# Performance work log

Measured on AMD Instinct MI355X. Metric: run time of the kernel, lower is better.

## Reference

```python
import jax, jax.numpy as jnp
import numpy as np

IN_C, OUT_C, P, K, STRIDE = 256, 256, 4, 3, 1
PAD = (K - 1) // 2

def setup_inputs() -> dict:
    key = jax.random.key(0)
    k1, k2, k3 = jax.random.split(key, 3)
    x = jax.random.normal(k1, (32, IN_C, 64, 64), dtype=jnp.float32)
    # KxK weights for (i,j) pairs where the KxK branch is taken
    Wk = jax.random.normal(k2, (OUT_C, IN_C, K, K), dtype=jnp.float32) * 0.05
    # 1x1 weights (one scalar per (i,j) pair) for the pointwise branch
    W1 = jax.random.normal(k3, (OUT_C, IN_C), dtype=jnp.float32) * 0.05
    return {"x": x, "Wk": Wk, "W1": W1}

def _effective_weight(Wk, W1):
    # Branch selection: j < first_K uses (in_c + j - first_K) % P == 0,
    # else (j - first_K) % P == 0; both equal (j - first_K) mod P == 0
    # with nonnegative modulo, where first_K = i % in_c.
    i = jnp.arange(OUT_C)[:, None]
    j = jnp.arange(IN_C)[None, :]
    first_K = i % IN_C
    kxk_mask = ((j - first_K) % P == 0)  # [out, in] bool
    # 1x1 conv (pad 0, stride s) == center tap of a padded KxK conv (pad (K-1)/2, stride s)
    center = jnp.zeros((K, K), Wk.dtype).at[K // 2, K // 2].set(1.0)
    W_1x1_embedded = W1[:, :, None, None] * center  # [out, in, K, K]
    return jnp.where(kxk_mask[:, :, None, None], Wk, W_1x1_embedded)

def reference(x, Wk, W1):
    W_eff = _effective_weight(Wk, W1)
    out = jax.lax.conv_general_dilated(
        x, W_eff,
        window_strides=(STRIDE, STRIDE),
        padding=[(PAD, PAD), (PAD, PAD)],
        dimension_numbers=("NCHW", "OIHW", "NCHW"),
    )
    return out
```

## Files before the change

kernel.cpp:

```cpp
#include <hip/hip_runtime.h>


#define IN_C  256
#define OUT_C 256
#define HH    64
#define WW    64

typedef __attribute__((ext_vector_type(8))) short   bf16x8;
typedef __attribute__((ext_vector_type(4))) float   f32x4;

__device__ __forceinline__ unsigned short f2bf(float f) {
    union { float f; unsigned int u; } v; v.f = f;
    unsigned int r = (v.u + 0x7FFFu + ((v.u >> 16) & 1u)) >> 16;
    return (unsigned short)r;
}

__global__ __launch_bounds__(256)
void hetconv_prep(const float* __restrict__ Wk, const float* __restrict__ W1,
                  unsigned short* __restrict__ ws16) {
    const int total = 81920 + 163840;
    for (int idx = blockIdx.x * 256 + threadIdx.x; idx < total; idx += gridDim.x * 256) {
        float f = 0.f;
        if (idx < 81920) {
            int i = idx % 40;
            int p = (idx / 40) & 255;
            int h = idx / 10240;
            int g = h & 3, h2 = h >> 2;
            if (i < 32) {
                int j  = g + 4 * (32 * h2 + i);
                int oc = 4 * (p & 63) + (p >> 6);
                f = ((p >> 6) == g) ? Wk[(oc * IN_C + j) * 9 + 4] : W1[oc * IN_C + j];
            }
        } else {
            int widx = idx - 81920;
            int i   = widx % 40;
            int lo  = (widx / 40) & 63;
            int tap = (widx / 2560) & 7;
            int h   = widx / 20480;
            int g = h & 3, h2 = h >> 2;
            if (i < 32) {
                int j  = g + 4 * (32 * h2 + i);
                int oc = 4 * lo + g;
                int tf = tap < 4 ? tap : tap + 1;
                f = Wk[(oc * IN_C + j) * 9 + tf];
            }
        }
        ws16[idx] = f2bf(f);
    }
}

__global__ __launch_bounds__(256, 2)
void hetconv_mfma(const float* __restrict__ x,
                  const unsigned short* __restrict__ wsw,
                  float* __restrict__ out) {
    __shared__ unsigned short xs[4 * 66 * 40];
    __shared__ unsigned short wh[256 * 40];
    __shared__ unsigned short wk[4 * 64 * 40];

    const int t    = threadIdx.x;
    const int l    = t & 63;
    const int w    = t >> 6;
    const int mrow = w & 1;
    const int ncol = w >> 1;
    const int lrow = l & 15;
    const int kc   = l >> 4;

    const int bid = blockIdx.x;
    const int n   = (bid & 7) * 4 + (bid >> 8);
    const int yt  = (bid >> 3) & 31;
    const int y0  = yt * 2;

    f32x4 acc[8][4];
    #pragma unroll
    for (int mi = 0; mi < 8; ++mi)
        #pragma unroll
        for (int ni = 0; ni < 4; ++ni) acc[mi][ni] = (f32x4){0.f, 0.f, 0.f, 0.f};

    if (t < 128) {
        int r = t >> 5, side = (t >> 4) & 1, icp = t & 15;
        *(unsigned int*)&xs[(r * 66 + side * 65) * 40 + icp * 2] = 0u;
    }

    for (int h2 = 0; h2 < 2; ++h2) {
        #pragma unroll
        for (int g = 0; g < 4; ++g) {
            const int h = h2 * 4 + g;
            __syncthreads();

            #pragma unroll
            for (int it = 0; it < 4; ++it) {
                int tau = t + it * 256;
                int icp = tau & 15;
                int q   = (tau >> 4) & 15;
                int r   = tau >> 8;
                int i0  = icp * 2;
                int j0  = g + 4 * (32 * h2 + i0);
                int gy  = y0 + r - 1;
                float4 v0 = {0.f, 0.f, 0.f, 0.f}, v1 = {0.f, 0.f, 0.f, 0.f};
                if ((unsigned)gy < 64u) {
                    const float* p0 = x + (((size_t)n * IN_C + j0) << 12) + (gy << 6) + q * 4;
                    v0 = *(const float4*)p0;
                    v1 = *(const float4*)(p0 + 4 * HH * WW);
                }
                unsigned int d0 = (unsigned)f2bf(v0.x) | ((unsigned)f2bf(v1.x) << 16);
                unsigned int d1 = (unsigned)f2bf(v0.y) | ((unsigned)f2bf(v1.y) << 16);
                unsigned int d2 = (unsigned)f2bf(v0.z) | ((unsigned)f2bf(v1.z) << 16);
                unsigned int d3 = (unsigned)f2bf(v0.w) | ((unsigned)f2bf(v1.w) << 16);
                int rb = (r * 66 + q * 4 + 1) * 40 + i0;
                *(unsigned int*)&xs[rb]           = d0;
                *(unsigned int*)&xs[rb + 40]      = d1;
                *(unsigned int*)&xs[rb + 80]      = d2;
                *(unsigned int*)&xs[rb + 120]     = d3;
            }
            {
                const unsigned short* hs = wsw + h * 10240;
                const unsigned short* ks = wsw + 81920 + h * 20480;
                #pragma unroll
                for (int it = 0; it < 5; ++it) {
                    int e = (t + it * 256) * 8;
                    *(bf16x8*)&wh[e] = *(const bf16x8*)&hs[e];
                    *(bf16x8*)&wk[e] = *(const bf16x8*)&ks[e];
                }
            }
            __syncthreads();

            {
                bf16x8 a[8], b[4];
                #pragma unroll
                for (int mi = 0; mi < 8; ++mi) {
                    int m = mrow + 2 * mi;
                    a[mi] = *(const bf16x8*)&wh[(m * 16 + lrow) * 40 + kc * 8];
                }
                #pragma unroll
                for (int ni = 0; ni < 4; ++ni)
                    b[ni] = *(const bf16x8*)&xs[((ncol + 1) * 66 + ni * 16 + lrow + 1) * 40 + kc * 8];
                #pragma unroll
                for (int mi = 0; mi < 8; ++mi)
                    #pragma unroll
                    for (int ni = 0; ni < 4; ++ni)
                        acc[mi][ni] = __builtin_amdgcn_mfma_f32_16x16x32_bf16(a[mi], b[ni], acc[mi][ni], 0, 0, 0);
            }

            #pragma unroll
            for (int tp = 0; tp < 4; ++tp) {
                const int tf = tp;
                const int dy = tf / 3 - 1, dx = tf % 3 - 1;
                bf16x8 a0 = *(const bf16x8*)&wk[(tp * 64 + mrow * 16 + lrow) * 40 + kc * 8];
                bf16x8 a1 = *(const bf16x8*)&wk[(tp * 64 + (mrow + 2) * 16 + lrow) * 40 + kc * 8];
                bf16x8 bb[4];
                #pragma unroll
                for (int ni = 0; ni < 4; ++ni)
                    bb[ni] = *(const bf16x8*)&xs[((ncol + 1 + dy) * 66 + ni * 16 + lrow + 1 + dx) * 40 + kc * 8];
                #pragma unroll
                for (int ni = 0; ni < 4; ++ni) {
                    acc[2 * g + 0][ni] = __builtin_amdgcn_mfma_f32_16x16x32_bf16(a0, bb[ni], acc[2 * g + 0][ni], 0, 0, 0);
                    acc[2 * g + 1][ni] = __builtin_amdgcn_mfma_f32_16x16x32_bf16(a1, bb[ni], acc[2 * g + 1][ni], 0, 0, 0);
                }
            }
            __syncthreads();

            {
                const unsigned short* ks = wsw + 81920 + h * 20480 + 10240;
                #pragma unroll
                for (int it = 0; it < 5; ++it) {
                    int e = (t + it * 256) * 8;
                    *(bf16x8*)&wk[e] = *(const bf16x8*)&ks[e];
                }
            }
            __syncthreads();

            #pragma unroll
            for (int tp = 0; tp < 4; ++tp) {
                const int tf = tp + 5;
                const int dy = tf / 3 - 1, dx = tf % 3 - 1;
                bf16x8 a0 = *(const bf16x8*)&wk[(tp * 64 + mrow * 16 + lrow) * 40 + kc * 8];
                bf16x8 a1 = *(const bf16x8*)&wk[(tp * 64 + (mrow + 2) * 16 + lrow) * 40 + kc * 8];
                bf16x8 bb[4];
                #pragma unroll
                for (int ni = 0; ni < 4; ++ni)
                    bb[ni] = *(const bf16x8*)&xs[((ncol + 1 + dy) * 66 + ni * 16 + lrow + 1 + dx) * 40 + kc * 8];
                #pragma unroll
                for (int ni = 0; ni < 4; ++ni) {
                    acc[2 * g + 0][ni] = __builtin_amdgcn_mfma_f32_16x16x32_bf16(a0, bb[ni], acc[2 * g + 0][ni], 0, 0, 0);
                    acc[2 * g + 1][ni] = __builtin_amdgcn_mfma_f32_16x16x32_bf16(a1, bb[ni], acc[2 * g + 1][ni], 0, 0, 0);
                }
            }
        }
    }

    #pragma unroll
    for (int mi = 0; mi < 8; ++mi) {
        int m = mrow + 2 * mi;
        #pragma unroll
        for (int ni = 0; ni < 4; ++ni) {
            #pragma unroll
            for (int reg = 0; reg < 4; ++reg) {
                int p  = m * 16 + kc * 4 + reg;
                int oc = 4 * (p & 63) + (p >> 6);
                out[(((size_t)n * OUT_C + oc) * HH + (y0 + ncol)) * WW + ni * 16 + lrow] = acc[mi][ni][reg];
            }
        }
    }
}

#define TH 16
#define TW 16
#define ICC 16
__global__ __launch_bounds__(256)
void hetconv_fp32(const float* __restrict__ x,
                  const float* __restrict__ Wk,
                  const float* __restrict__ W1,
                  float* __restrict__ out) {
    const int t    = threadIdx.x;
    const int g    = blockIdx.y;
    const int n    = blockIdx.z;
    const int tile = blockIdx.x;
    const int ty0  = (tile >> 2) * TH;
    const int tx0  = (tile & 3) * TW;
    const int ol = t & 7;
    const int pl = t >> 3;
    const int r  = pl >> 1;
    const int ch = (pl & 1) * 8;
    __shared__ __align__(16) float xsf[ICC * 18 * 20];
    __shared__ __align__(16) float w1s[ICC * 64];
    __shared__ __align__(16) float wks[4 * 9 * 64];
    float acc[8][8];
    #pragma unroll
    for (int k = 0; k < 8; ++k)
        #pragma unroll
        for (int p = 0; p < 8; ++p) acc[k][p] = 0.f;
    for (int ic0 = 0; ic0 < IN_C; ic0 += ICC) {
        for (int idx = t; idx < ICC * 18 * 18; idx += 256) {
            int ic = idx / 324, rem = idx - ic * 324, rr = rem / 18, cc = rem - rr * 18;
            int gy = ty0 + rr - 1, gx = tx0 + cc - 1;
            float v = 0.f;
            if (gy >= 0 && gy < HH && gx >= 0 && gx < WW)
                v = x[(((size_t)n * IN_C + ic0 + ic) * HH + gy) * WW + gx];
            xsf[ic * 360 + rr * 20 + cc] = v;
        }
        for (int idx = t; idx < ICC * 64; idx += 256) {
            int ic = idx >> 6, o = idx & 63;
            w1s[idx] = W1[(g + 4 * o) * IN_C + ic0 + ic];
        }
        for (int idx = t; idx < 4 * 9 * 64; idx += 256) {
            int a = idx / 576, rem = idx - a * 576, tap = rem >> 6, o = rem & 63;
            wks[idx] = Wk[((g + 4 * o) * IN_C + ic0 + g + 4 * a) * 9 + tap];
        }
        __syncthreads();
        for (int ic = 0; ic < ICC; ++ic) {
            if ((ic & 3) != g) {
                const float* rowp = &xsf[ic * 360 + (r + 1) * 20 + ch];
                float4 A = *(const float4*)rowp;
                float4 B = *(const float4*)(rowp + 4);
                float  c8 = rowp[8];
                float xv[8] = {A.y, A.z, A.w, B.x, B.y, B.z, B.w, c8};
                const float* wp = &w1s[ic * 64 + ol * 8];
                float4 wA = *(const float4*)wp;
                float4 wB = *(const float4*)(wp + 4);
                float wv[8] = {wA.x, wA.y, wA.z, wA.w, wB.x, wB.y, wB.z, wB.w};
                #pragma unroll
                for (int k = 0; k < 8; ++k)
                    #pragma unroll
                    for (int p = 0; p < 8; ++p) acc[k][p] += wv[k] * xv[p];
            } else {
                const int a = ic >> 2;
                #pragma unroll
                for (int dy = -1; dy <= 1; ++dy) {
                    const float* rowp = &xsf[ic * 360 + (r + 1 + dy) * 20 + ch];
                    float4 A = *(const float4*)rowp;
                    float4 B = *(const float4*)(rowp + 4);
                    float2 C = *(const float2*)(rowp + 8);
                    float seg[10] = {A.x, A.y, A.z, A.w, B.x, B.y, B.z, B.w, C.x, C.y};
                    #pragma unroll
                    for (int dxi = 0; dxi < 3; ++dxi) {
                        const float* wp = &wks[(a * 9 + (dy + 1) * 3 + dxi) * 64 + ol * 8];
                        float4 wA = *(const float4*)wp;
                        float4 wB = *(const float4*)(wp + 4);
                        float wv[8] = {wA.x, wA.y, wA.z, wA.w, wB.x, wB.y, wB.z, wB.w};
                        #pragma unroll
                        for (int k = 0; k < 8; ++k)
                            #pragma unroll
                            for (int p = 0; p < 8; ++p) acc[k][p] += wv[k] * seg[p + dxi];
                    }
                }
            }
        }
        __syncthreads();
    }
    #pragma unroll
    for (int k = 0; k < 8; ++k) {
        int oc = g + 4 * (ol * 8 + k);
        size_t base = (((size_t)n * OUT_C + oc) * HH + (ty0 + r)) * WW + tx0 + ch;
        float4 v0 = {acc[k][0], acc[k][1], acc[k][2], acc[k][3]};
        float4 v1 = {acc[k][4], acc[k][5], acc[k][6], acc[k][7]};
        *(float4*)(&out[base])     = v0;
        *(float4*)(&out[base + 4]) = v1;
    }
}

extern "C" void kernel_launch(void* const* d_in, const int* in_sizes, int n_in,
                              void* d_out, int out_size, void* d_ws, size_t ws_size,
                              hipStream_t stream) {
    const float* x  = (const float*)d_in[0];
    const float* Wk = (const float*)d_in[1];
    const float* W1 = (const float*)d_in[2];
    float* outp = (float*)d_out;

    if (ws_size >= (size_t)(81920 + 163840) * sizeof(unsigned short)) {
        hetconv_prep<<<240, 256, 0, stream>>>(Wk, W1, (unsigned short*)d_ws);
        hetconv_mfma<<<1024, 256, 0, stream>>>(x, (const unsigned short*)d_ws, outp);
    } else {
        hetconv_fp32<<<dim3(16, 4, 32), 256, 0, stream>>>(x, Wk, W1, outp);
    }
}
```

Measured before the change: 105.1 us.

## Double-buffer input tile in LDS and read weights straight from global

Weights are no longer staged through shared memory. The prep kernel now packs them into an MFMA-fragment order without padding, and the main kernel loads them directly from global/L2 memory. The input tile is double-buffered in LDS: the next channel chunk's global loads are issued before the current chunk's MFMAs and written afterwards, which overlaps memory latency with compute and cuts barriers from four per chunk to one. The risks are more register pressure from holding prefetched values, global-load latency on every weight fragment, and possible bank conflicts from the new 36-element LDS row pitch read with 8-byte loads.

```diff
diff --git a/kernel.cpp b/kernel.cpp
--- a/kernel.cpp
+++ b/kernel.cpp
@@ -6,8 +6,9 @@
 #define HH    64
 #define WW    64
 
-typedef __attribute__((ext_vector_type(8))) short   bf16x8;
-typedef __attribute__((ext_vector_type(4))) float   f32x4;
+typedef __attribute__((ext_vector_type(8))) short bf16x8;
+typedef __attribute__((ext_vector_type(4))) short bf16x4;
+typedef __attribute__((ext_vector_type(4))) float f32x4;
 
 __device__ __forceinline__ unsigned short f2bf(float f) {
     union { float f; unsigned int u; } v; v.f = f;
@@ -18,44 +19,119 @@
 __global__ __launch_bounds__(256)
 void hetconv_prep(const float* __restrict__ Wk, const float* __restrict__ W1,
                   unsigned short* __restrict__ ws16) {
-    const int total = 81920 + 163840;
-    for (int idx = blockIdx.x * 256 + threadIdx.x; idx < total; idx += gridDim.x * 256) {
-        float f = 0.f;
-        if (idx < 81920) {
-            int i = idx % 40;
-            int p = (idx / 40) & 255;
-            int h = idx / 10240;
+    const int TOTAL = 65536 + 131072;
+    for (int idx = blockIdx.x * 256 + threadIdx.x; idx < TOTAL; idx += gridDim.x * 256) {
+        float f;
+        if (idx < 65536) {
+            int e = idx & 7, kc = (idx >> 3) & 3, p = (idx >> 5) & 255, h = idx >> 13;
             int g = h & 3, h2 = h >> 2;
-            if (i < 32) {
-                int j  = g + 4 * (32 * h2 + i);
-                int oc = 4 * (p & 63) + (p >> 6);
-                f = ((p >> 6) == g) ? Wk[(oc * IN_C + j) * 9 + 4] : W1[oc * IN_C + j];
-            }
+            int i = kc * 8 + e;
+            int j = g + 4 * (32 * h2 + i);
+            int oc = 4 * (p & 63) + (p >> 6);
+            f = ((p >> 6) == g) ? Wk[(oc * IN_C + j) * 9 + 4] : W1[oc * IN_C + j];
         } else {
-            int widx = idx - 81920;
-            int i   = widx % 40;
-            int lo  = (widx / 40) & 63;
-            int tap = (widx / 2560) & 7;
-            int h   = widx / 20480;
+            int k = idx - 65536;
+            int e = k & 7, kc = (k >> 3) & 3, lo = (k >> 5) & 63, tf = (k >> 11) & 7, h = k >> 14;
             int g = h & 3, h2 = h >> 2;
-            if (i < 32) {
-                int j  = g + 4 * (32 * h2 + i);
-                int oc = 4 * lo + g;
-                int tf = tap < 4 ? tap : tap + 1;
-                f = Wk[(oc * IN_C + j) * 9 + tf];
-            }
+            int i = kc * 8 + e;
+            int j = g + 4 * (32 * h2 + i);
+            int oc = 4 * lo + g;
+            int tfull = tf < 4 ? tf : tf + 1;
+            f = Wk[(oc * IN_C + j) * 9 + tfull];
         }
         ws16[idx] = f2bf(f);
+    }
+}
+
+#define XSPAD 36
+#define XSSZ  (4 * 66 * XSPAD)
+
+__device__ __forceinline__ void stage_loads(const float* __restrict__ x, int n, int y0,
+                                            int ck, int t, float4 v[4][2]) {
+    const int g = ck & 3, h2 = ck >> 2;
+    #pragma unroll
+    for (int it = 0; it < 4; ++it) {
+        int tau = t + it * 256;
+        int icp = tau & 15, q = (tau >> 4) & 15, r = tau >> 8;
+        int i0 = icp * 2;
+        int j0 = g + 4 * (32 * h2 + i0);
+        int gy = y0 + r - 1;
+        float4 z = {0.f, 0.f, 0.f, 0.f};
+        v[it][0] = z; v[it][1] = z;
+        if ((unsigned)gy < 64u) {
+            const float* p0 = x + (((size_t)n * IN_C + j0) << 12) + (gy << 6) + (q << 2);
+            v[it][0] = *(const float4*)p0;
+            v[it][1] = *(const float4*)(p0 + 16384);
+        }
+    }
+}
+
+__device__ __forceinline__ void stage_writes(int t, float4 v[4][2], unsigned short* __restrict__ xb) {
+    #pragma unroll
+    for (int it = 0; it < 4; ++it) {
+        int tau = t + it * 256;
+        int icp = tau & 15, q = (tau >> 4) & 15, r = tau >> 8;
+        int i0 = icp * 2;
+        unsigned d0 = (unsigned)f2bf(v[it][0].x) | ((unsigned)f2bf(v[it][1].x) << 16);
+        unsigned d1 = (unsigned)f2bf(v[it][0].y) | ((unsigned)f2bf(v[it][1].y) << 16);
+        unsigned d2 = (unsigned)f2bf(v[it][0].z) | ((unsigned)f2bf(v[it][1].z) << 16);
+        unsigned d3 = (unsigned)f2bf(v[it][0].w) | ((unsigned)f2bf(v[it][1].w) << 16);
+        int rb = (r * 66 + q * 4 + 1) * XSPAD + i0;
+        *(unsigned*)&xb[rb]             = d0;
+        *(unsigned*)&xb[rb + XSPAD]     = d1;
+        *(unsigned*)&xb[rb + 2 * XSPAD] = d2;
+        *(unsigned*)&xb[rb + 3 * XSPAD] = d3;
+    }
+}
+
+__device__ __forceinline__ bf16x8 lds_bfrag(const unsigned short* __restrict__ xb, int off) {
+    bf16x4 lo = *(const bf16x4*)&xb[off];
+    bf16x4 hi = *(const bf16x4*)&xb[off + 4];
+    return __builtin_shufflevector(lo, hi, 0, 1, 2, 3, 4, 5, 6, 7);
+}
+
+template <int G>
+__device__ __forceinline__ void compute_chunk(int ck,
+        const unsigned short* __restrict__ AH, const unsigned short* __restrict__ AK,
+        const unsigned short* __restrict__ xb, f32x4 acc[8][4],
+        int mrow, int ncol, int lrow, int kc) {
+    const unsigned short* AHh = AH + (ck << 13);
+    const unsigned short* AKh = AK + (ck << 14);
+
+    bf16x8 bfr[4];
+    #pragma unroll
+    for (int ni = 0; ni < 4; ++ni)
+        bfr[ni] = lds_bfrag(xb, ((ncol + 1) * 66 + ni * 16 + lrow + 1) * XSPAD + kc * 8);
+    #pragma unroll
+    for (int mi = 0; mi < 8; ++mi) {
+        int m = mrow + 2 * mi;
+        bf16x8 a = *(const bf16x8*)&AHh[((m * 16 + lrow) * 4 + kc) * 8];
+        #pragma unroll
+        for (int ni = 0; ni < 4; ++ni)
+            acc[mi][ni] = __builtin_amdgcn_mfma_f32_16x16x32_bf16(a, bfr[ni], acc[mi][ni], 0, 0, 0);
+    }
+
+    #pragma unroll
+    for (int tf = 0; tf < 8; ++tf) {
+        const int tfull = tf < 4 ? tf : tf + 1;
+        const int dy = tfull / 3 - 1, dx = tfull % 3 - 1;
+        const unsigned short* ak = &AKh[((tf * 64 + mrow * 16 + lrow) * 4 + kc) * 8];
+        bf16x8 a0 = *(const bf16x8*)ak;
+        bf16x8 a1 = *(const bf16x8*)(ak + 1024);
+        #pragma unroll
+        for (int ni = 0; ni < 4; ++ni) {
+            bf16x8 bb = lds_bfrag(xb, ((ncol + 1 + dy) * 66 + ni * 16 + lrow + 1 + dx) * XSPAD + kc * 8);
+            acc[2 * G + 0][ni] = __builtin_amdgcn_mfma_f32_16x16x32_bf16(a0, bb, acc[2 * G + 0][ni], 0, 0, 0);
+            acc[2 * G + 1][ni] = __builtin_amdgcn_mfma_f32_16x16x32_bf16(a1, bb, acc[2 * G + 1][ni], 0, 0, 0);
+        }
     }
 }
 
 __global__ __launch_bounds__(256, 2)
 void hetconv_mfma(const float* __restrict__ x,
-                  const unsigned short* __restrict__ wsw,
+                  const unsigned short* __restrict__ wgt,
                   float* __restrict__ out) {
-    __shared__ unsigned short xs[4 * 66 * 40];
-    __shared__ unsigned short wh[256 * 40];
-    __shared__ unsigned short wk[4 * 64 * 40];
+    __shared__ __align__(16) unsigned short xs[2][XSSZ];
 
     const int t    = threadIdx.x;
     const int l    = t & 63;
@@ -67,8 +143,10 @@
 
     const int bid = blockIdx.x;
     const int n   = (bid & 7) * 4 + (bid >> 8);
-    const int yt  = (bid >> 3) & 31;
-    const int y0  = yt * 2;
+    const int y0  = ((bid >> 3) & 31) * 2;
+
+    const unsigned short* AH = wgt;
+    const unsigned short* AK = wgt + 65536;
 
     f32x4 acc[8][4];
     #pragma unroll
@@ -76,116 +154,29 @@
         #pragma unroll
         for (int ni = 0; ni < 4; ++ni) acc[mi][ni] = (f32x4){0.f, 0.f, 0.f, 0.f};
 
-    if (t < 128) {
-        int r = t >> 5, side = (t >> 4) & 1, icp = t & 15;
-        *(unsigned int*)&xs[(r * 66 + side * 65) * 40 + icp * 2] = 0u;
-    }
-
+    {
+        float4 v[4][2];
+        stage_loads(x, n, y0, 0, t, v);
+        int buf = t >> 7, r = (t >> 5) & 3, side = (t >> 4) & 1, u = t & 15;
+        *(unsigned*)&xs[buf][(r * 66 + side * 65) * XSPAD + u * 2] = 0u;
+        stage_writes(t, v, xs[0]);
+        __syncthreads();
+    }
+
+    #pragma unroll 1
     for (int h2 = 0; h2 < 2; ++h2) {
-        #pragma unroll
-        for (int g = 0; g < 4; ++g) {
-            const int h = h2 * 4 + g;
-            __syncthreads();
-
-            #pragma unroll
-            for (int it = 0; it < 4; ++it) {
-                int tau = t + it * 256;
-                int icp = tau & 15;
-                int q   = (tau >> 4) & 15;
-                int r   = tau >> 8;
-                int i0  = icp * 2;
-                int j0  = g + 4 * (32 * h2 + i0);
-                int gy  = y0 + r - 1;
-                float4 v0 = {0.f, 0.f, 0.f, 0.f}, v1 = {0.f, 0.f, 0.f, 0.f};
-                if ((unsigned)gy < 64u) {
-                    const float* p0 = x + (((size_t)n * IN_C + j0) << 12) + (gy << 6) + q * 4;
-                    v0 = *(const float4*)p0;
-                    v1 = *(const float4*)(p0 + 4 * HH * WW);
-                }
-                unsigned int d0 = (unsigned)f2bf(v0.x) | ((unsigned)f2bf(v1.x) << 16);
-                unsigned int d1 = (unsigned)f2bf(v0.y) | ((unsigned)f2bf(v1.y) << 16);
-                unsigned int d2 = (unsigned)f2bf(v0.z) | ((unsigned)f2bf(v1.z) << 16);
-                unsigned int d3 = (unsigned)f2bf(v0.w) | ((unsigned)f2bf(v1.w) << 16);
-                int rb = (r * 66 + q * 4 + 1) * 40 + i0;
-                *(unsigned int*)&xs[rb]           = d0;
-                *(unsigned int*)&xs[rb + 40]      = d1;
-                *(unsigned int*)&xs[rb + 80]      = d2;
-                *(unsigned int*)&xs[rb + 120]     = d3;
-            }
-            {
-                const unsigned short* hs = wsw + h * 10240;
-                const unsigned short* ks = wsw + 81920 + h * 20480;
-                #pragma unroll
-                for (int it = 0; it < 5; ++it) {
-                    int e = (t + it * 256) * 8;
-                    *(bf16x8*)&wh[e] = *(const bf16x8*)&hs[e];
-                    *(bf16x8*)&wk[e] = *(const bf16x8*)&ks[e];
-                }
-            }
-            __syncthreads();
-
-            {
-                bf16x8 a[8], b[4];
-                #pragma unroll
-                for (int mi = 0; mi < 8; ++mi) {
-                    int m = mrow + 2 * mi;
-                    a[mi] = *(const bf16x8*)&wh[(m * 16 + lrow) * 40 + kc * 8];
-                }
-                #pragma unroll
-                for (int ni = 0; ni < 4; ++ni)
-                    b[ni] = *(const bf16x8*)&xs[((ncol + 1) * 66 + ni * 16 + lrow + 1) * 40 + kc * 8];
-                #pragma unroll
-                for (int mi = 0; mi < 8; ++mi)
-                    #pragma unroll
-                    for (int ni = 0; ni < 4; ++ni)
-                        acc[mi][ni] = __builtin_amdgcn_mfma_f32_16x16x32_bf16(a[mi], b[ni], acc[mi][ni], 0, 0, 0);
-            }
-
-            #pragma unroll
-            for (int tp = 0; tp < 4; ++tp) {
-                const int tf = tp;
-                const int dy = tf / 3 - 1, dx = tf % 3 - 1;
-                bf16x8 a0 = *(const bf16x8*)&wk[(tp * 64 + mrow * 16 + lrow) * 40 + kc * 8];
-                bf16x8 a1 = *(const bf16x8*)&wk[(tp * 64 + (mrow + 2) * 16 + lrow) * 40 + kc * 8];
-                bf16x8 bb[4];
-                #pragma unroll
-                for (int ni = 0; ni < 4; ++ni)
-                    bb[ni] = *(const bf16x8*)&xs[((ncol + 1 + dy) * 66 + ni * 16 + lrow + 1 + dx) * 40 + kc * 8];
-                #pragma unroll
-                for (int ni = 0; ni < 4; ++ni) {
-                    acc[2 * g + 0][ni] = __builtin_amdgcn_mfma_f32_16x16x32_bf16(a0, bb[ni], acc[2 * g + 0][ni], 0, 0, 0);
-                    acc[2 * g + 1][ni] = __builtin_amdgcn_mfma_f32_16x16x32_bf16(a1, bb[ni], acc[2 * g + 1][ni], 0, 0, 0);
-                }
-            }
-            __syncthreads();
-
-            {
-                const unsigned short* ks = wsw + 81920 + h * 20480 + 10240;
-                #pragma unroll
-                for (int it = 0; it < 5; ++it) {
-                    int e = (t + it * 256) * 8;
-                    *(bf16x8*)&wk[e] = *(const bf16x8*)&ks[e];
-                }
-            }
-            __syncthreads();
-
-            #pragma unroll
-            for (int tp = 0; tp < 4; ++tp) {
-                const int tf = tp + 5;
-                const int dy = tf / 3 - 1, dx = tf % 3 - 1;
-                bf16x8 a0 = *(const bf16x8*)&wk[(tp * 64 + mrow * 16 + lrow) * 40 + kc * 8];
-                bf16x8 a1 = *(const bf16x8*)&wk[(tp * 64 + (mrow + 2) * 16 + lrow) * 40 + kc * 8];
-                bf16x8 bb[4];
-                #pragma unroll
-                for (int ni = 0; ni < 4; ++ni)
-                    bb[ni] = *(const bf16x8*)&xs[((ncol + 1 + dy) * 66 + ni * 16 + lrow + 1 + dx) * 40 + kc * 8];
-                #pragma unroll
-                for (int ni = 0; ni < 4; ++ni) {
-                    acc[2 * g + 0][ni] = __builtin_amdgcn_mfma_f32_16x16x32_bf16(a0, bb[ni], acc[2 * g + 0][ni], 0, 0, 0);
-                    acc[2 * g + 1][ni] = __builtin_amdgcn_mfma_f32_16x16x32_bf16(a1, bb[ni], acc[2 * g + 1][ni], 0, 0, 0);
-                }
-            }
-        }
+#define BODY(G)                                                                  \
+        {                                                                        \
+            const int ck = h2 * 4 + G;                                           \
+            const int nc = ck + 1;                                               \
+            float4 nv[4][2];                                                     \
+            if (G < 3 || h2 == 0) stage_loads(x, n, y0, nc, t, nv);              \
+            compute_chunk<G>(ck, AH, AK, xs[G & 1], acc, mrow, ncol, lrow, kc);  \
+            if (G < 3 || h2 == 0) stage_writes(t, nv, xs[(G + 1) & 1]);          \
+            __syncthreads();                                                     \
+        }
+        BODY(0) BODY(1) BODY(2) BODY(3)
+#undef BODY
     }
 
     #pragma unroll
@@ -306,8 +297,8 @@
     const float* W1 = (const float*)d_in[2];
     float* outp = (float*)d_out;
 
-    if (ws_size >= (size_t)(81920 + 163840) * sizeof(unsigned short)) {
-        hetconv_prep<<<240, 256, 0, stream>>>(Wk, W1, (unsigned short*)d_ws);
+    if (ws_size >= (size_t)(65536 + 131072) * sizeof(unsigned short)) {
+        hetconv_prep<<<256, 256, 0, stream>>>(Wk, W1, (unsigned short*)d_ws);
         hetconv_mfma<<<1024, 256, 0, stream>>>(x, (const unsigned short*)d_ws, outp);
     } else {
         hetconv_fp32<<<dim3(16, 4, 32), 256, 0, stream>>>(x, Wk, W1, outp);
```

After: 169.1 us. 1.61x slower.

## Software-pipeline global loads of x and weights into registers across chunks

Applied to the files above, without the earlier changes.

Restructures the MFMA kernel's main loop into eight fully unrolled chunks. The global loads for the next chunk's x tile and the second half of the KxK weights are issued into registers before the current MFMA work, so their latency overlaps with compute. Float-to-bf16 packing now uses the HIP intrinsic __float22bfloat162_rn in place of manual bit manipulation. The cost is higher register pressure from the prefetch buffers, which could hurt occupancy under launch_bounds(256,2).

```diff
diff --git a/kernel.cpp b/kernel.cpp
--- a/kernel.cpp
+++ b/kernel.cpp
@@ -1,4 +1,5 @@
 #include <hip/hip_runtime.h>
+#include <hip/hip_bf16.h>
 
 
 #define IN_C  256
@@ -6,13 +7,19 @@
 #define HH    64
 #define WW    64
 
-typedef __attribute__((ext_vector_type(8))) short   bf16x8;
-typedef __attribute__((ext_vector_type(4))) float   f32x4;
+typedef __attribute__((ext_vector_type(8))) short bf16x8;
+typedef __attribute__((ext_vector_type(4))) float f32x4;
 
 __device__ __forceinline__ unsigned short f2bf(float f) {
     union { float f; unsigned int u; } v; v.f = f;
     unsigned int r = (v.u + 0x7FFFu + ((v.u >> 16) & 1u)) >> 16;
     return (unsigned short)r;
+}
+
+__device__ __forceinline__ unsigned pkbf(float lo, float hi) {
+    union { __hip_bfloat162 b; unsigned u; } c;
+    c.b = __float22bfloat162_rn(make_float2(lo, hi));
+    return c.u;
 }
 
 __global__ __launch_bounds__(256)
@@ -49,6 +56,44 @@
     }
 }
 
+__device__ __forceinline__ void stage_x_loads(const float* __restrict__ x, int n, int y0,
+                                              int ck, int t, float4 v[4][2]) {
+    const int g = ck & 3, h2 = ck >> 2;
+    #pragma unroll
+    for (int it = 0; it < 4; ++it) {
+        int tau = t + it * 256;
+        int icp = tau & 15, q = (tau >> 4) & 15, r = tau >> 8;
+        int i0 = icp * 2;
+        int j0 = g + 4 * (32 * h2 + i0);
+        int gy = y0 + r - 1;
+        float4 z = {0.f, 0.f, 0.f, 0.f};
+        v[it][0] = z; v[it][1] = z;
+        if ((unsigned)gy < 64u) {
+            const float* p0 = x + (((size_t)n * IN_C + j0) << 12) + (gy << 6) + (q << 2);
+            v[it][0] = *(const float4*)p0;
+            v[it][1] = *(const float4*)(p0 + 16384);
+        }
+    }
+}
+
+__device__ __forceinline__ void stage_x_writes(int t, float4 v[4][2], unsigned short* __restrict__ xb) {
+    #pragma unroll
+    for (int it = 0; it < 4; ++it) {
+        int tau = t + it * 256;
+        int icp = tau & 15, q = (tau >> 4) & 15, r = tau >> 8;
+        int i0 = icp * 2;
+        unsigned d0 = pkbf(v[it][0].x, v[it][1].x);
+        unsigned d1 = pkbf(v[it][0].y, v[it][1].y);
+        unsigned d2 = pkbf(v[it][0].z, v[it][1].z);
+        unsigned d3 = pkbf(v[it][0].w, v[it][1].w);
+        int rb = (r * 66 + q * 4 + 1) * 40 + i0;
+        *(unsigned*)&xb[rb]        = d0;
+        *(unsigned*)&xb[rb + 40]   = d1;
+        *(unsigned*)&xb[rb + 80]   = d2;
+        *(unsigned*)&xb[rb + 120]  = d3;
+    }
+}
+
 __global__ __launch_bounds__(256, 2)
 void hetconv_mfma(const float* __restrict__ x,
                   const unsigned short* __restrict__ wsw,
@@ -67,8 +112,7 @@
 
     const int bid = blockIdx.x;
     const int n   = (bid & 7) * 4 + (bid >> 8);
-    const int yt  = (bid >> 3) & 31;
-    const int y0  = yt * 2;
+    const int y0  = ((bid >> 3) & 31) * 2;
 
     f32x4 acc[8][4];
     #pragma unroll
@@ -77,116 +121,94 @@
         for (int ni = 0; ni < 4; ++ni) acc[mi][ni] = (f32x4){0.f, 0.f, 0.f, 0.f};
 
     if (t < 128) {
-        int r = t >> 5, side = (t >> 4) & 1, icp = t & 15;
-        *(unsigned int*)&xs[(r * 66 + side * 65) * 40 + icp * 2] = 0u;
-    }
-
-    for (int h2 = 0; h2 < 2; ++h2) {
-        #pragma unroll
-        for (int g = 0; g < 4; ++g) {
-            const int h = h2 * 4 + g;
-            __syncthreads();
-
-            #pragma unroll
-            for (int it = 0; it < 4; ++it) {
-                int tau = t + it * 256;
-                int icp = tau & 15;
-                int q   = (tau >> 4) & 15;
-                int r   = tau >> 8;
-                int i0  = icp * 2;
-                int j0  = g + 4 * (32 * h2 + i0);
-                int gy  = y0 + r - 1;
-                float4 v0 = {0.f, 0.f, 0.f, 0.f}, v1 = {0.f, 0.f, 0.f, 0.f};
-                if ((unsigned)gy < 64u) {
-                    const float* p0 = x + (((size_t)n * IN_C + j0) << 12) + (gy << 6) + q * 4;
-                    v0 = *(const float4*)p0;
-                    v1 = *(const float4*)(p0 + 4 * HH * WW);
-                }
-                unsigned int d0 = (unsigned)f2bf(v0.x) | ((unsigned)f2bf(v1.x) << 16);
-                unsigned int d1 = (unsigned)f2bf(v0.y) | ((unsigned)f2bf(v1.y) << 16);
-                unsigned int d2 = (unsigned)f2bf(v0.z) | ((unsigned)f2bf(v1.z) << 16);
-                unsigned int d3 = (unsigned)f2bf(v0.w) | ((unsigned)f2bf(v1.w) << 16);
-                int rb = (r * 66 + q * 4 + 1) * 40 + i0;
-                *(unsigned int*)&xs[rb]           = d0;
-                *(unsigned int*)&xs[rb + 40]      = d1;
-                *(unsigned int*)&xs[rb + 80]      = d2;
-                *(unsigned int*)&xs[rb + 120]     = d3;
-            }
-            {
-                const unsigned short* hs = wsw + h * 10240;
-                const unsigned short* ks = wsw + 81920 + h * 20480;
-                #pragma unroll
-                for (int it = 0; it < 5; ++it) {
-                    int e = (t + it * 256) * 8;
-                    *(bf16x8*)&wh[e] = *(const bf16x8*)&hs[e];
-                    *(bf16x8*)&wk[e] = *(const bf16x8*)&ks[e];
-                }
-            }
-            __syncthreads();
-
-            {
-                bf16x8 a[8], b[4];
-                #pragma unroll
-                for (int mi = 0; mi < 8; ++mi) {
-                    int m = mrow + 2 * mi;
-                    a[mi] = *(const bf16x8*)&wh[(m * 16 + lrow) * 40 + kc * 8];
-                }
-                #pragma unroll
-                for (int ni = 0; ni < 4; ++ni)
-                    b[ni] = *(const bf16x8*)&xs[((ncol + 1) * 66 + ni * 16 + lrow + 1) * 40 + kc * 8];
-                #pragma unroll
-                for (int mi = 0; mi < 8; ++mi)
-                    #pragma unroll
-                    for (int ni = 0; ni < 4; ++ni)
-                        acc[mi][ni] = __builtin_amdgcn_mfma_f32_16x16x32_bf16(a[mi], b[ni], acc[mi][ni], 0, 0, 0);
-            }
-
-            #pragma unroll
-            for (int tp = 0; tp < 4; ++tp) {
-                const int tf = tp;
-                const int dy = tf / 3 - 1, dx = tf % 3 - 1;
-                bf16x8 a0 = *(const bf16x8*)&wk[(tp * 64 + mrow * 16 + lrow) * 40 + kc * 8];
-                bf16x8 a1 = *(const bf16x8*)&wk[(tp * 64 + (mrow + 2) * 16 + lrow) * 40 + kc * 8];
-                bf16x8 bb[4];
-                #pragma unroll
-                for (int ni = 0; ni < 4; ++ni)
-                    bb[ni] = *(const bf16x8*)&xs[((ncol + 1 + dy) * 66 + ni * 16 + lrow + 1 + dx) * 40 + kc * 8];
-                #pragma unroll
-                for (int ni = 0; ni < 4; ++ni) {
-                    acc[2 * g + 0][ni] = __builtin_amdgcn_mfma_f32_16x16x32_bf16(a0, bb[ni], acc[2 * g + 0][ni], 0, 0, 0);
-                    acc[2 * g + 1][ni] = __builtin_amdgcn_mfma_f32_16x16x32_bf16(a1, bb[ni], acc[2 * g + 1][ni], 0, 0, 0);
-                }
-            }
-            __syncthreads();
-
-            {
-                const unsigned short* ks = wsw + 81920 + h * 20480 + 10240;
-                #pragma unroll
-                for (int it = 0; it < 5; ++it) {
-                    int e = (t + it * 256) * 8;
-                    *(bf16x8*)&wk[e] = *(const bf16x8*)&ks[e];
-                }
-            }
-            __syncthreads();
-
-            #pragma unroll
-            for (int tp = 0; tp < 4; ++tp) {
-                const int tf = tp + 5;
-                const int dy = tf / 3 - 1, dx = tf % 3 - 1;
-                bf16x8 a0 = *(const bf16x8*)&wk[(tp * 64 + mrow * 16 + lrow) * 40 + kc * 8];
-                bf16x8 a1 = *(const bf16x8*)&wk[(tp * 64 + (mrow + 2) * 16 + lrow) * 40 + kc * 8];
-                bf16x8 bb[4];
-                #pragma unroll
-                for (int ni = 0; ni < 4; ++ni)
-                    bb[ni] = *(const bf16x8*)&xs[((ncol + 1 + dy) * 66 + ni * 16 + lrow + 1 + dx) * 40 + kc * 8];
-                #pragma unroll
-                for (int ni = 0; ni < 4; ++ni) {
-                    acc[2 * g + 0][ni] = __builtin_amdgcn_mfma_f32_16x16x32_bf16(a0, bb[ni], acc[2 * g + 0][ni], 0, 0, 0);
-                    acc[2 * g + 1][ni] = __builtin_amdgcn_mfma_f32_16x16x32_bf16(a1, bb[ni], acc[2 * g + 1][ni], 0, 0, 0);
-                }
-            }
-        }
-    }
+        int r = t >> 5, side = (t >> 4) & 1, u = t & 15;
+        *(unsigned*)&xs[(r * 66 + side * 65) * 40 + u * 2] = 0u;
+    }
+    float4 xv[4][2];
+    stage_x_loads(x, n, y0, 0, t, xv);
+
+#define CHUNK(CK, LAST)                                                             \
+    {                                                                               \
+        const unsigned short* hs = wsw + (CK) * 10240;                              \
+        const unsigned short* ks = wsw + 81920 + (CK) * 20480;                      \
+        __syncthreads();                          \
+        bf16x8 wv[10];                                                              \
+        _Pragma("unroll")                                                           \
+        for (int it = 0; it < 5; ++it) {          \
+            int e = (t + it * 256) * 8;                                             \
+            wv[it]     = *(const bf16x8*)&hs[e];                                    \
+            wv[5 + it] = *(const bf16x8*)&ks[e];                                    \
+        }                                                                           \
+        stage_x_writes(t, xv, xs);               \
+        _Pragma("unroll")                                                           \
+        for (int it = 0; it < 5; ++it) {                                            \
+            int e = (t + it * 256) * 8;                                             \
+            *(bf16x8*)&wh[e] = wv[it];                                              \
+            *(bf16x8*)&wk[e] = wv[5 + it];                                          \
+        }                                                                           \
+        __syncthreads();                                 \
+        bf16x8 wvb[5];                                                              \
+        _Pragma("unroll")                                                           \
+        for (int it = 0; it < 5; ++it)             \
+            wvb[it] = *(const bf16x8*)&ks[10240 + (t + it * 256) * 8];              \
+        {                                        \
+            bf16x8 a[8], b[4];                                                      \
+            _Pragma("unroll")                                                       \
+            for (int mi = 0; mi < 8; ++mi) {                                        \
+                int m = mrow + 2 * mi;                                              \
+                a[mi] = *(const bf16x8*)&wh[(m * 16 + lrow) * 40 + kc * 8];         \
+            }                                                                       \
+            _Pragma("unroll")                                                       \
+            for (int ni = 0; ni < 4; ++ni)                                          \
+                b[ni] = *(const bf16x8*)&xs[((ncol + 1) * 66 + ni * 16 + lrow + 1) * 40 + kc * 8]; \
+            _Pragma("unroll")                                                       \
+            for (int mi = 0; mi < 8; ++mi)                                          \
+                _Pragma("unroll")                                                   \
+                for (int ni = 0; ni < 4; ++ni)                                      \
+                    acc[mi][ni] = __builtin_amdgcn_mfma_f32_16x16x32_bf16(a[mi], b[ni], acc[mi][ni], 0, 0, 0); \
+        }                                                                           \
+        {                                      \
+            constexpr int G = (CK) & 3;                                             \
+            _Pragma("unroll")                                                       \
+            for (int tp = 0; tp < 4; ++tp) {                                        \
+                const int dy = tp / 3 - 1, dx = tp % 3 - 1;                         \
+                bf16x8 a0 = *(const bf16x8*)&wk[(tp * 64 + mrow * 16 + lrow) * 40 + kc * 8]; \
+                bf16x8 a1 = *(const bf16x8*)&wk[(tp * 64 + (mrow + 2) * 16 + lrow) * 40 + kc * 8]; \
+                _Pragma("unroll")                                                   \
+                for (int ni = 0; ni < 4; ++ni) {                                    \
+                    bf16x8 bb = *(const bf16x8*)&xs[((ncol + 1 + dy) * 66 + ni * 16 + lrow + 1 + dx) * 40 + kc * 8]; \
+                    acc[2 * G + 0][ni] = __builtin_amdgcn_mfma_f32_16x16x32_bf16(a0, bb, acc[2 * G + 0][ni], 0, 0, 0); \
+                    acc[2 * G + 1][ni] = __builtin_amdgcn_mfma_f32_16x16x32_bf16(a1, bb, acc[2 * G + 1][ni], 0, 0, 0); \
+                }                                                                   \
+            }                                                                       \
+        }                                                                           \
+        __syncthreads();                                    \
+        _Pragma("unroll")                                                           \
+        for (int it = 0; it < 5; ++it)                                              \
+            *(bf16x8*)&wk[(t + it * 256) * 8] = wvb[it];                            \
+        if (!(LAST)) stage_x_loads(x, n, y0, (CK) + 1, t, xv);   \
+        __syncthreads();                                         \
+        {                                      \
+            constexpr int G = (CK) & 3;                                             \
+            _Pragma("unroll")                                                       \
+            for (int tp = 0; tp < 4; ++tp) {                                        \
+                const int tf = tp + 5;                                              \
+                const int dy = tf / 3 - 1, dx = tf % 3 - 1;                         \
+                bf16x8 a0 = *(const bf16x8*)&wk[(tp * 64 + mrow * 16 + lrow) * 40 + kc * 8]; \
+                bf16x8 a1 = *(const bf16x8*)&wk[(tp * 64 + (mrow + 2) * 16 + lrow) * 40 + kc * 8]; \
+                _Pragma("unroll")                                                   \
+                for (int ni = 0; ni < 4; ++ni) {                                    \
+                    bf16x8 bb = *(const bf16x8*)&xs[((ncol + 1 + dy) * 66 + ni * 16 + lrow + 1 + dx) * 40 + kc * 8]; \
+                    acc[2 * G + 0][ni] = __builtin_amdgcn_mfma_f32_16x16x32_bf16(a0, bb, acc[2 * G + 0][ni], 0, 0, 0); \
+                    acc[2 * G + 1][ni] = __builtin_amdgcn_mfma_f32_16x16x32_bf16(a1, bb, acc[2 * G + 1][ni], 0, 0, 0); \
+                }                                                                   \
+            }                                                                       \
+        }                                                                           \
+    }
+
+    CHUNK(0, 0) CHUNK(1, 0) CHUNK(2, 0) CHUNK(3, 0)
+    CHUNK(4, 0) CHUNK(5, 0) CHUNK(6, 0) CHUNK(7, 1)
+#undef CHUNK
 
     #pragma unroll
     for (int mi = 0; mi < 8; ++mi) {
@@ -223,7 +245,7 @@
     const int ch = (pl & 1) * 8;
     __shared__ __align__(16) float xsf[ICC * 18 * 20];
     __shared__ __align__(16) float w1s[ICC * 64];
-    __shared__ __align__(16) float wks[4 * 9 * 64];
+    __shared__ __align__(16) float wksf[4 * 9 * 64];
     float acc[8][8];
     #pragma unroll
     for (int k = 0; k < 8; ++k)
@@ -244,7 +266,7 @@
         }
         for (int idx = t; idx < 4 * 9 * 64; idx += 256) {
             int a = idx / 576, rem = idx - a * 576, tap = rem >> 6, o = rem & 63;
-            wks[idx] = Wk[((g + 4 * o) * IN_C + ic0 + g + 4 * a) * 9 + tap];
+            wksf[idx] = Wk[((g + 4 * o) * IN_C + ic0 + g + 4 * a) * 9 + tap];
         }
         __syncthreads();
         for (int ic = 0; ic < ICC; ++ic) {
@@ -253,15 +275,15 @@
                 float4 A = *(const float4*)rowp;
                 float4 B = *(const float4*)(rowp + 4);
                 float  c8 = rowp[8];
-                float xv[8] = {A.y, A.z, A.w, B.x, B.y, B.z, B.w, c8};
+                float xv2[8] = {A.y, A.z, A.w, B.x, B.y, B.z, B.w, c8};
                 const float* wp = &w1s[ic * 64 + ol * 8];
                 float4 wA = *(const float4*)wp;
                 float4 wB = *(const float4*)(wp + 4);
-                float wv[8] = {wA.x, wA.y, wA.z, wA.w, wB.x, wB.y, wB.z, wB.w};
+                float wv2[8] = {wA.x, wA.y, wA.z, wA.w, wB.x, wB.y, wB.z, wB.w};
                 #pragma unroll
                 for (int k = 0; k < 8; ++k)
                     #pragma unroll
-                    for (int p = 0; p < 8; ++p) acc[k][p] += wv[k] * xv[p];
+                    for (int p = 0; p < 8; ++p) acc[k][p] += wv2[k] * xv2[p];
             } else {
                 const int a = ic >> 2;
                 #pragma unroll
@@ -273,14 +295,14 @@
                     float seg[10] = {A.x, A.y, A.z, A.w, B.x, B.y, B.z, B.w, C.x, C.y};
                     #pragma unroll
                     for (int dxi = 0; dxi < 3; ++dxi) {
-                        const float* wp = &wks[(a * 9 + (dy + 1) * 3 + dxi) * 64 + ol * 8];
+                        const float* wp = &wksf[(a * 9 + (dy + 1) * 3 + dxi) * 64 + ol * 8];
                         float4 wA = *(const float4*)wp;
                         float4 wB = *(const float4*)(wp + 4);
-                        float wv[8] = {wA.x, wA.y, wA.z, wA.w, wB.x, wB.y, wB.z, wB.w};
+                        float wv2[8] = {wA.x, wA.y, wA.z, wA.w, wB.x, wB.y, wB.z, wB.w};
                         #pragma unroll
                         for (int k = 0; k < 8; ++k)
                             #pragma unroll
-                            for (int p = 0; p < 8; ++p) acc[k][p] += wv[k] * seg[p + dxi];
+                            for (int p = 0; p < 8; ++p) acc[k][p] += wv2[k] * seg[p + dxi];
                     }
                 }
             }
```

Result: faster. 101.2 us, median of 2 (-3.8%).
